# Kernel optimization log

Hardware: AMD Instinct MI355X
Metric: run time of the kernel (lower is better)

The kernel has to match this reference:

```python
import jax, jax.numpy as jnp
import numpy as np

M = 262144          # rows of A == prod(out_shape) == 512*512
N = 262144          # cols of A == prod(x.shape)
NNZ = 8388608       # 32 nonzeros per row on average
OUT_SHAPE = (512, 512)


def setup_inputs() -> dict:
    key = jax.random.key(0)
    k1, k2, k3, k4 = jax.random.split(key, 4)
    A_rows = jax.random.randint(k1, (NNZ,), 0, M, dtype=jnp.int32)
    A_cols = jax.random.randint(k2, (NNZ,), 0, N, dtype=jnp.int32)
    A_vals = jax.random.normal(k3, (NNZ,), dtype=jnp.float32)
    x = jax.random.normal(k4, OUT_SHAPE, dtype=jnp.float32)
    return {"x": x, "A_vals": A_vals, "A_rows": A_rows, "A_cols": A_cols}


def reference(x, A_vals, A_rows, A_cols):
    # x.reshape(A.shape[1], 1); torch.sparse.mm(A, x); reshape(out_shape)
    xf = x.reshape(-1)                                   # [N]
    contrib = A_vals * jnp.take(xf, A_cols)              # [NNZ] gather + multiply
    y = jax.ops.segment_sum(contrib, A_rows, num_segments=M)  # scatter-add over rows
    return y.reshape(OUT_SHAPE).astype(jnp.float32)
```

## Files before the change

### kernel.cpp

```cpp
#include <hip/hip_runtime.h>


#define BINS         32
#define ROW_SHIFT    13
#define ROWS_PER_BIN 8192
#define ENT          4096
#define CUR_STRIDE   32
#define SLICES       16

typedef int   __attribute__((ext_vector_type(4))) i32x4;
typedef float __attribute__((ext_vector_type(4))) f32x4;


__global__ __launch_bounds__(256) void zero_out_kernel(float* __restrict__ y, int n) {
    int i = blockIdx.x * blockDim.x + threadIdx.x;
    if (i < n) y[i] = 0.0f;
}

__global__ __launch_bounds__(256) void spmv_coo_scatter(
    const float* __restrict__ vals, const int* __restrict__ rows,
    const int* __restrict__ cols, const float* __restrict__ x,
    float* __restrict__ y, int nnz)
{
    int i = (blockIdx.x * blockDim.x + threadIdx.x) * 4;
    if (i + 3 < nnz) {
        float4 v = *reinterpret_cast<const float4*>(vals + i);
        int4   r = *reinterpret_cast<const int4*>(rows + i);
        int4   c = *reinterpret_cast<const int4*>(cols + i);
        atomicAdd(&y[r.x], v.x * x[c.x]);
        atomicAdd(&y[r.y], v.y * x[c.y]);
        atomicAdd(&y[r.z], v.z * x[c.z]);
        atomicAdd(&y[r.w], v.w * x[c.w]);
    } else {
        for (; i < nnz; ++i) atomicAdd(&y[rows[i]], vals[i] * x[cols[i]]);
    }
}


__global__ __launch_bounds__(256) void init_cursors(unsigned* __restrict__ gcur, int n) {
    int i = blockIdx.x * 256 + threadIdx.x;
    if (i < n) gcur[i] = 0u;
}

__global__ __launch_bounds__(256) void scatter2_kernel(
    const int*   __restrict__ rows, const int* __restrict__ cols,
    const float* __restrict__ vals, const float* __restrict__ x, int nnz,
    unsigned* __restrict__ gcur, unsigned cap,
    unsigned short* __restrict__ okeys, float* __restrict__ ocontrib)
{
    __shared__ unsigned cnt[BINS];
    __shared__ int      dstb[BINS];
    __shared__ unsigned cur2[BINS];
    __shared__ unsigned total_s;
    __shared__ unsigned short skey[ENT];
    __shared__ float          sval[ENT];
    __shared__ unsigned char  sbin[ENT];

    const int t = threadIdx.x;
    if (t < BINS) cnt[t] = 0u;
    __syncthreads();

    const int seg = blockIdx.x * ENT;

    int   rr[16];
    int   cc[16];
    float ff[16];

    if (seg + ENT <= nnz) {
        #pragma unroll
        for (int ch = 0; ch < 4; ++ch) {
            int base = seg + ch * 1024 + t * 4;
            i32x4 r4 = *reinterpret_cast<const i32x4*>(rows + base);
            i32x4 c4 = *reinterpret_cast<const i32x4*>(cols + base);
            f32x4 v4 = *reinterpret_cast<const f32x4*>(vals + base);
            rr[ch*4+0] = r4.x; cc[ch*4+0] = c4.x; ff[ch*4+0] = v4.x;
            rr[ch*4+1] = r4.y; cc[ch*4+1] = c4.y; ff[ch*4+1] = v4.y;
            rr[ch*4+2] = r4.z; cc[ch*4+2] = c4.z; ff[ch*4+2] = v4.z;
            rr[ch*4+3] = r4.w; cc[ch*4+3] = c4.w; ff[ch*4+3] = v4.w;
        }
        #pragma unroll
        for (int j = 0; j < 16; ++j) ff[j] *= x[cc[j]];
    } else {
        #pragma unroll
        for (int ch = 0; ch < 4; ++ch) {
            #pragma unroll
            for (int j = 0; j < 4; ++j) {
                int idx = seg + ch * 1024 + t * 4 + j;
                if (idx < nnz) { rr[ch*4+j] = rows[idx]; cc[ch*4+j] = cols[idx]; ff[ch*4+j] = vals[idx]; }
                else           { rr[ch*4+j] = -1; cc[ch*4+j] = 0; ff[ch*4+j] = 0.0f; }
            }
        }
        #pragma unroll
        for (int j = 0; j < 16; ++j) if (rr[j] >= 0) ff[j] *= x[cc[j]];
    }

    #pragma unroll
    for (int j = 0; j < 16; ++j)
        if (rr[j] >= 0) atomicAdd(&cnt[rr[j] >> ROW_SHIFT], 1u);
    __syncthreads();

    if (t < BINS) {
        unsigned c = cnt[t];
        unsigned resv = atomicAdd(&gcur[t * CUR_STRIDE], c);
        unsigned v = c;
        #pragma unroll
        for (int d = 1; d < BINS; d <<= 1) {
            unsigned o = __shfl_up(v, d, 64);
            if (t >= d) v += o;
        }
        unsigned ls = v - c;
        cur2[t] = ls;
        dstb[t] = (int)resv - (int)ls;
        if (t == BINS - 1) total_s = v;
    }
    __syncthreads();

    #pragma unroll
    for (int j = 0; j < 16; ++j) {
        if (rr[j] >= 0) {
            int b = rr[j] >> ROW_SHIFT;
            unsigned p = atomicAdd(&cur2[b], 1u);
            skey[p] = (unsigned short)(rr[j] & (ROWS_PER_BIN - 1));
            sval[p] = ff[j];
            sbin[p] = (unsigned char)b;
        }
    }
    __syncthreads();

    const unsigned total = total_s;
    for (unsigned i = t; i < total; i += 256) {
        int b = sbin[i];
        unsigned off = (unsigned)(dstb[b] + (int)i);
        if (off < cap) {
            size_t dst = (size_t)b * cap + off;
            okeys[dst]    = skey[i];
            ocontrib[dst] = sval[i];
        }
    }
}

__global__ __launch_bounds__(512) void accum2_kernel(
    const unsigned short* __restrict__ okeys, const float* __restrict__ ocontrib,
    const unsigned* __restrict__ gcur, unsigned cap,
    float* __restrict__ partials)
{
    __shared__ float acc[ROWS_PER_BIN];
    const int t   = threadIdx.x;
    const int bin = blockIdx.x / SLICES;
    const int sl  = blockIdx.x - bin * SLICES;

    float4 z = make_float4(0.f, 0.f, 0.f, 0.f);
    #pragma unroll
    for (int i = 0; i < ROWS_PER_BIN / (512 * 4); ++i)
        *reinterpret_cast<float4*>(&acc[(i * 512 + t) * 4]) = z;
    __syncthreads();

    unsigned count = gcur[bin * CUR_STRIDE];
    if (count > cap) count = cap;
    unsigned chunk = ((count + SLICES - 1u) / SLICES + 3u) & ~3u;
    unsigned lo = (unsigned)sl * chunk;
    unsigned hi = lo + chunk; if (hi > count) hi = count;

    const unsigned short* k = okeys    + (size_t)bin * cap;
    const float*          c = ocontrib + (size_t)bin * cap;

    unsigned i = lo + (unsigned)t * 4u;

    for (; i + 6147u < hi; i += 8192u) {
        ushort4 k0 = *reinterpret_cast<const ushort4*>(k + i);
        ushort4 k1 = *reinterpret_cast<const ushort4*>(k + i + 2048u);
        ushort4 k2 = *reinterpret_cast<const ushort4*>(k + i + 4096u);
        ushort4 k3 = *reinterpret_cast<const ushort4*>(k + i + 6144u);
        float4  c0 = *reinterpret_cast<const float4*>(c + i);
        float4  c1 = *reinterpret_cast<const float4*>(c + i + 2048u);
        float4  c2 = *reinterpret_cast<const float4*>(c + i + 4096u);
        float4  c3 = *reinterpret_cast<const float4*>(c + i + 6144u);
        atomicAdd(&acc[k0.x], c0.x); atomicAdd(&acc[k0.y], c0.y);
        atomicAdd(&acc[k0.z], c0.z); atomicAdd(&acc[k0.w], c0.w);
        atomicAdd(&acc[k1.x], c1.x); atomicAdd(&acc[k1.y], c1.y);
        atomicAdd(&acc[k1.z], c1.z); atomicAdd(&acc[k1.w], c1.w);
        atomicAdd(&acc[k2.x], c2.x); atomicAdd(&acc[k2.y], c2.y);
        atomicAdd(&acc[k2.z], c2.z); atomicAdd(&acc[k2.w], c2.w);
        atomicAdd(&acc[k3.x], c3.x); atomicAdd(&acc[k3.y], c3.y);
        atomicAdd(&acc[k3.z], c3.z); atomicAdd(&acc[k3.w], c3.w);
    }
    for (; i + 3u < hi; i += 2048u) {
        ushort4 k4 = *reinterpret_cast<const ushort4*>(k + i);
        float4  c4 = *reinterpret_cast<const float4*>(c + i);
        atomicAdd(&acc[k4.x], c4.x);
        atomicAdd(&acc[k4.y], c4.y);
        atomicAdd(&acc[k4.z], c4.z);
        atomicAdd(&acc[k4.w], c4.w);
    }
    for (; i < hi; ++i) atomicAdd(&acc[k[i]], c[i]);
    __syncthreads();

    float* p = partials + (size_t)blockIdx.x * ROWS_PER_BIN;
    #pragma unroll
    for (int i2 = 0; i2 < ROWS_PER_BIN / (512 * 4); ++i2) {
        int l = (i2 * 512 + t) * 4;
        *reinterpret_cast<float4*>(p + l) = *reinterpret_cast<const float4*>(&acc[l]);
    }
}

__global__ __launch_bounds__(256) void reduce2_kernel(
    const float* __restrict__ partials, float* __restrict__ y, int out_size)
{
    int r0 = (blockIdx.x * 256 + threadIdx.x) * 4;
    if (r0 >= out_size) return;
    int bin = r0 >> ROW_SHIFT, local = r0 & (ROWS_PER_BIN - 1);
    const float* p = partials + ((size_t)bin * SLICES) * ROWS_PER_BIN + local;
    float4 s = make_float4(0.f, 0.f, 0.f, 0.f);
    #pragma unroll
    for (int j = 0; j < SLICES; ++j) {
        float4 v = *reinterpret_cast<const float4*>(p + (size_t)j * ROWS_PER_BIN);
        s.x += v.x; s.y += v.y; s.z += v.z; s.w += v.w;
    }
    *reinterpret_cast<float4*>(y + r0) = s;
}

extern "C" void kernel_launch(void* const* d_in, const int* in_sizes, int n_in,
                              void* d_out, int out_size, void* d_ws, size_t ws_size,
                              hipStream_t stream) {
    const float* x    = (const float*)d_in[0];
    const float* vals = (const float*)d_in[1];
    const int*   rows = (const int*)d_in[2];
    const int*   cols = (const int*)d_in[3];
    float* y = (float*)d_out;

    const int nnz  = in_sizes[1];
    const int bins = (out_size + ROWS_PER_BIN - 1) / ROWS_PER_BIN;

    unsigned cap = (unsigned)(nnz / (bins > 0 ? bins : 1)) + 16384u;
    cap = (cap + 3u) & ~3u;

    auto align256 = [](size_t v) { return (v + 255) & ~(size_t)255; };

    size_t off_contrib  = 0;
    size_t off_keys     = align256(off_contrib + (size_t)BINS * cap * 4);
    size_t off_partials = align256(off_keys + (size_t)BINS * cap * 2);
    size_t off_gcur     = align256(off_partials + (size_t)BINS * SLICES * ROWS_PER_BIN * 4);
    size_t need         = align256(off_gcur + (size_t)BINS * CUR_STRIDE * 4);

    const bool ok = (bins == BINS) && (need <= ws_size) && (nnz > 0) &&
                    (out_size == BINS * ROWS_PER_BIN);

    if (!ok) {
        zero_out_kernel<<<(out_size + 255) / 256, 256, 0, stream>>>(y, out_size);
        spmv_coo_scatter<<<(nnz + 1023) / 1024, 256, 0, stream>>>(vals, rows, cols, x, y, nnz);
        return;
    }

    char* w = (char*)d_ws;
    float*          ocontrib = (float*)(w + off_contrib);
    unsigned short* okeys    = (unsigned short*)(w + off_keys);
    float*          partials = (float*)(w + off_partials);
    unsigned*       gcur     = (unsigned*)(w + off_gcur);

    const int ncur = BINS * CUR_STRIDE;
    init_cursors<<<(ncur + 255) / 256, 256, 0, stream>>>(gcur, ncur);
    scatter2_kernel<<<(nnz + ENT - 1) / ENT, 256, 0, stream>>>(
        rows, cols, vals, x, nnz, gcur, cap, okeys, ocontrib);
    accum2_kernel<<<BINS * SLICES, 512, 0, stream>>>(okeys, ocontrib, gcur, cap, partials);
    reduce2_kernel<<<(out_size / 4 + 255) / 256, 256, 0, stream>>>(partials, y, out_size);
}
```

Baseline: 217.3 us.

## Fuse scatter, accumulate and reduce into one persistent kernel with grid barriers

Replaces the three separate kernels (bin scatter, per-bin shared-memory accumulation, partial reduction) with a single persistent kernel of BINS*SL blocks that loops over segments, then uses software grid-wide barriers between phases. The shared-memory staging buffer and the accumulator are placed in a union. Slices per bin rise from 16 to 32 when the workspace allows. This removes launch gaps and tail effects between stages. In exchange, the grid is capped at 1024 blocks of 256 threads for the scatter phase, the spin barrier depends on all blocks being co-resident, and the accumulate phase now runs with 256 threads per block instead of 512. The final reduce is scalar and sums 32 partials per output.

```diff
diff --git a/kernel.cpp b/kernel.cpp
--- a/kernel.cpp
+++ b/kernel.cpp
@@ -6,10 +6,9 @@
 #define ROWS_PER_BIN 8192
 #define ENT          4096
 #define CUR_STRIDE   32
-#define SLICES       16
-
-typedef int   __attribute__((ext_vector_type(4))) i32x4;
-typedef float __attribute__((ext_vector_type(4))) f32x4;
+
+typedef int   i32x4 __attribute__((ext_vector_type(4)));
+typedef float f32x4 __attribute__((ext_vector_type(4)));
 
 
 __global__ __launch_bounds__(256) void zero_out_kernel(float* __restrict__ y, int n) {
@@ -37,186 +36,214 @@
 }
 
 
-__global__ __launch_bounds__(256) void init_cursors(unsigned* __restrict__ gcur, int n) {
+__global__ __launch_bounds__(256) void init_kernel(
+    unsigned* __restrict__ gcur, int ncur, unsigned* __restrict__ bar)
+{
     int i = blockIdx.x * 256 + threadIdx.x;
-    if (i < n) gcur[i] = 0u;
-}
-
-__global__ __launch_bounds__(256) void scatter2_kernel(
+    if (i < ncur) gcur[i] = 0u;
+    if (blockIdx.x == 0 && threadIdx.x < 2) bar[threadIdx.x] = 0u;
+}
+
+__device__ __forceinline__ void grid_sync(unsigned* bar, unsigned nb) {
+    __syncthreads();
+    if (threadIdx.x == 0) {
+        __threadfence();
+        unsigned g = __hip_atomic_load(&bar[1], __ATOMIC_RELAXED, __HIP_MEMORY_SCOPE_AGENT);
+        unsigned a = __hip_atomic_fetch_add(&bar[0], 1u, __ATOMIC_ACQ_REL, __HIP_MEMORY_SCOPE_AGENT);
+        if (a + 1u == nb) {
+            __hip_atomic_store(&bar[0], 0u, __ATOMIC_RELAXED, __HIP_MEMORY_SCOPE_AGENT);
+            __hip_atomic_fetch_add(&bar[1], 1u, __ATOMIC_RELEASE, __HIP_MEMORY_SCOPE_AGENT);
+        } else {
+            while (__hip_atomic_load(&bar[1], __ATOMIC_ACQUIRE, __HIP_MEMORY_SCOPE_AGENT) == g)
+                __builtin_amdgcn_s_sleep(8);
+        }
+        __threadfence();
+    }
+    __syncthreads();
+}
+
+template <int SL>
+__global__ __launch_bounds__(256, 4) void mega_kernel(
     const int*   __restrict__ rows, const int* __restrict__ cols,
     const float* __restrict__ vals, const float* __restrict__ x, int nnz,
     unsigned* __restrict__ gcur, unsigned cap,
-    unsigned short* __restrict__ okeys, float* __restrict__ ocontrib)
+    unsigned short* __restrict__ okeys, float* __restrict__ ocontrib,
+    float* __restrict__ partials, float* __restrict__ y,
+    unsigned* __restrict__ bar, int out_size)
 {
-    __shared__ unsigned cnt[BINS];
-    __shared__ int      dstb[BINS];
-    __shared__ unsigned cur2[BINS];
-    __shared__ unsigned total_s;
-    __shared__ unsigned short skey[ENT];
-    __shared__ float          sval[ENT];
-    __shared__ unsigned char  sbin[ENT];
-
-    const int t = threadIdx.x;
-    if (t < BINS) cnt[t] = 0u;
-    __syncthreads();
-
-    const int seg = blockIdx.x * ENT;
-
-    int   rr[16];
-    int   cc[16];
-    float ff[16];
-
-    if (seg + ENT <= nnz) {
+    __shared__ union {
+        struct {
+            unsigned short skey[ENT];
+            float          sval[ENT];
+            unsigned char  sbin[ENT];
+            unsigned cnt[BINS];
+            int      dstb[BINS];
+            unsigned cur2[BINS];
+            unsigned total;
+        } s;
+        float acc[ROWS_PER_BIN];
+    } sm;
+
+    const int t    = threadIdx.x;
+    const int blk  = blockIdx.x;
+    const int grid = BINS * SL;
+    const int nseg = (nnz + ENT - 1) / ENT;
+
+    for (int s = blk; s < nseg; s += grid) {
+        __syncthreads();
+        if (t < BINS) sm.s.cnt[t] = 0u;
+        __syncthreads();
+
+        const int seg = s * ENT;
+        int   rr[16];
+        int   cc[16];
+        float ff[16];
+
+        if (seg + ENT <= nnz) {
+            #pragma unroll
+            for (int ch = 0; ch < 4; ++ch) {
+                int base = seg + ch * 1024 + t * 4;
+                i32x4 r4 = *reinterpret_cast<const i32x4*>(rows + base);
+                i32x4 c4 = *reinterpret_cast<const i32x4*>(cols + base);
+                f32x4 v4 = *reinterpret_cast<const f32x4*>(vals + base);
+                rr[ch*4+0] = r4.x; cc[ch*4+0] = c4.x; ff[ch*4+0] = v4.x;
+                rr[ch*4+1] = r4.y; cc[ch*4+1] = c4.y; ff[ch*4+1] = v4.y;
+                rr[ch*4+2] = r4.z; cc[ch*4+2] = c4.z; ff[ch*4+2] = v4.z;
+                rr[ch*4+3] = r4.w; cc[ch*4+3] = c4.w; ff[ch*4+3] = v4.w;
+            }
+            #pragma unroll
+            for (int j = 0; j < 16; ++j) ff[j] *= x[cc[j]];
+        } else {
+            #pragma unroll
+            for (int ch = 0; ch < 4; ++ch) {
+                #pragma unroll
+                for (int j = 0; j < 4; ++j) {
+                    int idx = seg + ch * 1024 + t * 4 + j;
+                    if (idx < nnz) { rr[ch*4+j] = rows[idx]; cc[ch*4+j] = cols[idx]; ff[ch*4+j] = vals[idx]; }
+                    else           { rr[ch*4+j] = -1; cc[ch*4+j] = 0; ff[ch*4+j] = 0.0f; }
+                }
+            }
+            #pragma unroll
+            for (int j = 0; j < 16; ++j) if (rr[j] >= 0) ff[j] *= x[cc[j]];
+        }
+
         #pragma unroll
-        for (int ch = 0; ch < 4; ++ch) {
-            int base = seg + ch * 1024 + t * 4;
-            i32x4 r4 = *reinterpret_cast<const i32x4*>(rows + base);
-            i32x4 c4 = *reinterpret_cast<const i32x4*>(cols + base);
-            f32x4 v4 = *reinterpret_cast<const f32x4*>(vals + base);
-            rr[ch*4+0] = r4.x; cc[ch*4+0] = c4.x; ff[ch*4+0] = v4.x;
-            rr[ch*4+1] = r4.y; cc[ch*4+1] = c4.y; ff[ch*4+1] = v4.y;
-            rr[ch*4+2] = r4.z; cc[ch*4+2] = c4.z; ff[ch*4+2] = v4.z;
-            rr[ch*4+3] = r4.w; cc[ch*4+3] = c4.w; ff[ch*4+3] = v4.w;
-        }
+        for (int j = 0; j < 16; ++j)
+            if (rr[j] >= 0) atomicAdd(&sm.s.cnt[rr[j] >> ROW_SHIFT], 1u);
+        __syncthreads();
+
+        if (t < BINS) {
+            unsigned c = sm.s.cnt[t];
+            unsigned resv = atomicAdd(&gcur[t * CUR_STRIDE], c);
+            unsigned v = c;
+            #pragma unroll
+            for (int d = 1; d < BINS; d <<= 1) {
+                unsigned o = __shfl_up(v, d, 64);
+                if (t >= d) v += o;
+            }
+            unsigned ls = v - c;
+            sm.s.cur2[t] = ls;
+            sm.s.dstb[t] = (int)resv - (int)ls;
+            if (t == BINS - 1) sm.s.total = v;
+        }
+        __syncthreads();
+
         #pragma unroll
-        for (int j = 0; j < 16; ++j) ff[j] *= x[cc[j]];
-    } else {
+        for (int j = 0; j < 16; ++j) {
+            if (rr[j] >= 0) {
+                int b = rr[j] >> ROW_SHIFT;
+                unsigned p = atomicAdd(&sm.s.cur2[b], 1u);
+                sm.s.skey[p] = (unsigned short)(rr[j] & (ROWS_PER_BIN - 1));
+                sm.s.sval[p] = ff[j];
+                sm.s.sbin[p] = (unsigned char)b;
+            }
+        }
+        __syncthreads();
+
+        const unsigned total = sm.s.total;
+        for (unsigned i = t; i < total; i += 256) {
+            int b = sm.s.sbin[i];
+            unsigned off = (unsigned)(sm.s.dstb[b] + (int)i);
+            if (off < cap) {
+                size_t dst = (size_t)b * cap + off;
+                okeys[dst]    = sm.s.skey[i];
+                ocontrib[dst] = sm.s.sval[i];
+            }
+        }
+    }
+
+    grid_sync(bar, (unsigned)grid);
+
+    {
+        const int bin = blk / SL;
+        const int sl  = blk - bin * SL;
+
+        float4 z = make_float4(0.f, 0.f, 0.f, 0.f);
         #pragma unroll
-        for (int ch = 0; ch < 4; ++ch) {
-            #pragma unroll
-            for (int j = 0; j < 4; ++j) {
-                int idx = seg + ch * 1024 + t * 4 + j;
-                if (idx < nnz) { rr[ch*4+j] = rows[idx]; cc[ch*4+j] = cols[idx]; ff[ch*4+j] = vals[idx]; }
-                else           { rr[ch*4+j] = -1; cc[ch*4+j] = 0; ff[ch*4+j] = 0.0f; }
-            }
-        }
+        for (int i = 0; i < ROWS_PER_BIN / (256 * 4); ++i)
+            *reinterpret_cast<float4*>(&sm.acc[(i * 256 + t) * 4]) = z;
+        __syncthreads();
+
+        unsigned count = gcur[bin * CUR_STRIDE];
+        if (count > cap) count = cap;
+        unsigned chunk = ((count + (unsigned)SL - 1u) / (unsigned)SL + 3u) & ~3u;
+        unsigned lo = (unsigned)sl * chunk;
+        unsigned hi = lo + chunk; if (hi > count) hi = count;
+
+        const unsigned short* k = okeys    + (size_t)bin * cap;
+        const float*          c = ocontrib + (size_t)bin * cap;
+
+        unsigned i = lo + (unsigned)t * 4u;
+
+        for (; i + 7171u < hi; i += 8192u) {
+            ushort4 K[8];
+            float4  C[8];
+            #pragma unroll
+            for (int j = 0; j < 8; ++j) K[j] = *reinterpret_cast<const ushort4*>(k + i + (unsigned)j * 1024u);
+            #pragma unroll
+            for (int j = 0; j < 8; ++j) C[j] = *reinterpret_cast<const float4*>(c + i + (unsigned)j * 1024u);
+            #pragma unroll
+            for (int j = 0; j < 8; ++j) {
+                atomicAdd(&sm.acc[K[j].x], C[j].x);
+                atomicAdd(&sm.acc[K[j].y], C[j].y);
+                atomicAdd(&sm.acc[K[j].z], C[j].z);
+                atomicAdd(&sm.acc[K[j].w], C[j].w);
+            }
+        }
+        for (; i + 3u < hi; i += 1024u) {
+            ushort4 k4 = *reinterpret_cast<const ushort4*>(k + i);
+            float4  c4 = *reinterpret_cast<const float4*>(c + i);
+            atomicAdd(&sm.acc[k4.x], c4.x);
+            atomicAdd(&sm.acc[k4.y], c4.y);
+            atomicAdd(&sm.acc[k4.z], c4.z);
+            atomicAdd(&sm.acc[k4.w], c4.w);
+        }
+        for (; i < hi; ++i) atomicAdd(&sm.acc[k[i]], c[i]);
+        __syncthreads();
+
+        float* p = partials + (size_t)blk * ROWS_PER_BIN;
         #pragma unroll
-        for (int j = 0; j < 16; ++j) if (rr[j] >= 0) ff[j] *= x[cc[j]];
-    }
-
-    #pragma unroll
-    for (int j = 0; j < 16; ++j)
-        if (rr[j] >= 0) atomicAdd(&cnt[rr[j] >> ROW_SHIFT], 1u);
-    __syncthreads();
-
-    if (t < BINS) {
-        unsigned c = cnt[t];
-        unsigned resv = atomicAdd(&gcur[t * CUR_STRIDE], c);
-        unsigned v = c;
-        #pragma unroll
-        for (int d = 1; d < BINS; d <<= 1) {
-            unsigned o = __shfl_up(v, d, 64);
-            if (t >= d) v += o;
-        }
-        unsigned ls = v - c;
-        cur2[t] = ls;
-        dstb[t] = (int)resv - (int)ls;
-        if (t == BINS - 1) total_s = v;
-    }
-    __syncthreads();
-
-    #pragma unroll
-    for (int j = 0; j < 16; ++j) {
-        if (rr[j] >= 0) {
-            int b = rr[j] >> ROW_SHIFT;
-            unsigned p = atomicAdd(&cur2[b], 1u);
-            skey[p] = (unsigned short)(rr[j] & (ROWS_PER_BIN - 1));
-            sval[p] = ff[j];
-            sbin[p] = (unsigned char)b;
-        }
-    }
-    __syncthreads();
-
-    const unsigned total = total_s;
-    for (unsigned i = t; i < total; i += 256) {
-        int b = sbin[i];
-        unsigned off = (unsigned)(dstb[b] + (int)i);
-        if (off < cap) {
-            size_t dst = (size_t)b * cap + off;
-            okeys[dst]    = skey[i];
-            ocontrib[dst] = sval[i];
-        }
-    }
-}
-
-__global__ __launch_bounds__(512) void accum2_kernel(
-    const unsigned short* __restrict__ okeys, const float* __restrict__ ocontrib,
-    const unsigned* __restrict__ gcur, unsigned cap,
-    float* __restrict__ partials)
-{
-    __shared__ float acc[ROWS_PER_BIN];
-    const int t   = threadIdx.x;
-    const int bin = blockIdx.x / SLICES;
-    const int sl  = blockIdx.x - bin * SLICES;
-
-    float4 z = make_float4(0.f, 0.f, 0.f, 0.f);
-    #pragma unroll
-    for (int i = 0; i < ROWS_PER_BIN / (512 * 4); ++i)
-        *reinterpret_cast<float4*>(&acc[(i * 512 + t) * 4]) = z;
-    __syncthreads();
-
-    unsigned count = gcur[bin * CUR_STRIDE];
-    if (count > cap) count = cap;
-    unsigned chunk = ((count + SLICES - 1u) / SLICES + 3u) & ~3u;
-    unsigned lo = (unsigned)sl * chunk;
-    unsigned hi = lo + chunk; if (hi > count) hi = count;
-
-    const unsigned short* k = okeys    + (size_t)bin * cap;
-    const float*          c = ocontrib + (size_t)bin * cap;
-
-    unsigned i = lo + (unsigned)t * 4u;
-
-    for (; i + 6147u < hi; i += 8192u) {
-        ushort4 k0 = *reinterpret_cast<const ushort4*>(k + i);
-        ushort4 k1 = *reinterpret_cast<const ushort4*>(k + i + 2048u);
-        ushort4 k2 = *reinterpret_cast<const ushort4*>(k + i + 4096u);
-        ushort4 k3 = *reinterpret_cast<const ushort4*>(k + i + 6144u);
-        float4  c0 = *reinterpret_cast<const float4*>(c + i);
-        float4  c1 = *reinterpret_cast<const float4*>(c + i + 2048u);
-        float4  c2 = *reinterpret_cast<const float4*>(c + i + 4096u);
-        float4  c3 = *reinterpret_cast<const float4*>(c + i + 6144u);
-        atomicAdd(&acc[k0.x], c0.x); atomicAdd(&acc[k0.y], c0.y);
-        atomicAdd(&acc[k0.z], c0.z); atomicAdd(&acc[k0.w], c0.w);
-        atomicAdd(&acc[k1.x], c1.x); atomicAdd(&acc[k1.y], c1.y);
-        atomicAdd(&acc[k1.z], c1.z); atomicAdd(&acc[k1.w], c1.w);
-        atomicAdd(&acc[k2.x], c2.x); atomicAdd(&acc[k2.y], c2.y);
-        atomicAdd(&acc[k2.z], c2.z); atomicAdd(&acc[k2.w], c2.w);
-        atomicAdd(&acc[k3.x], c3.x); atomicAdd(&acc[k3.y], c3.y);
-        atomicAdd(&acc[k3.z], c3.z); atomicAdd(&acc[k3.w], c3.w);
-    }
-    for (; i + 3u < hi; i += 2048u) {
-        ushort4 k4 = *reinterpret_cast<const ushort4*>(k + i);
-        float4  c4 = *reinterpret_cast<const float4*>(c + i);
-        atomicAdd(&acc[k4.x], c4.x);
-        atomicAdd(&acc[k4.y], c4.y);
-        atomicAdd(&acc[k4.z], c4.z);
-        atomicAdd(&acc[k4.w], c4.w);
-    }
-    for (; i < hi; ++i) atomicAdd(&acc[k[i]], c[i]);
-    __syncthreads();
-
-    float* p = partials + (size_t)blockIdx.x * ROWS_PER_BIN;
-    #pragma unroll
-    for (int i2 = 0; i2 < ROWS_PER_BIN / (512 * 4); ++i2) {
-        int l = (i2 * 512 + t) * 4;
-        *reinterpret_cast<float4*>(p + l) = *reinterpret_cast<const float4*>(&acc[l]);
-    }
-}
-
-__global__ __launch_bounds__(256) void reduce2_kernel(
-    const float* __restrict__ partials, float* __restrict__ y, int out_size)
-{
-    int r0 = (blockIdx.x * 256 + threadIdx.x) * 4;
-    if (r0 >= out_size) return;
-    int bin = r0 >> ROW_SHIFT, local = r0 & (ROWS_PER_BIN - 1);
-    const float* p = partials + ((size_t)bin * SLICES) * ROWS_PER_BIN + local;
-    float4 s = make_float4(0.f, 0.f, 0.f, 0.f);
-    #pragma unroll
-    for (int j = 0; j < SLICES; ++j) {
-        float4 v = *reinterpret_cast<const float4*>(p + (size_t)j * ROWS_PER_BIN);
-        s.x += v.x; s.y += v.y; s.z += v.z; s.w += v.w;
-    }
-    *reinterpret_cast<float4*>(y + r0) = s;
+        for (int i2 = 0; i2 < ROWS_PER_BIN / (256 * 4); ++i2) {
+            int l = (i2 * 256 + t) * 4;
+            *reinterpret_cast<float4*>(p + l) = *reinterpret_cast<const float4*>(&sm.acc[l]);
+        }
+    }
+
+    grid_sync(bar, (unsigned)grid);
+
+    {
+        const int rpb = out_size / grid;
+        const int r0  = blk * rpb;
+        for (int r = r0 + t; r < r0 + rpb; r += 256) {
+            int bin   = r >> ROW_SHIFT;
+            int local = r & (ROWS_PER_BIN - 1);
+            const float* p = partials + ((size_t)bin * SL) * ROWS_PER_BIN + local;
+            float ssum = 0.0f;
+            #pragma unroll
+            for (int j = 0; j < SL; ++j) ssum += p[(size_t)j * ROWS_PER_BIN];
+            y[r] = ssum;
+        }
+    }
 }
 
 extern "C" void kernel_launch(void* const* d_in, const int* in_sizes, int n_in,
@@ -236,11 +263,18 @@
 
     auto align256 = [](size_t v) { return (v + 255) & ~(size_t)255; };
 
-    size_t off_contrib  = 0;
-    size_t off_keys     = align256(off_contrib + (size_t)BINS * cap * 4);
-    size_t off_partials = align256(off_keys + (size_t)BINS * cap * 2);
-    size_t off_gcur     = align256(off_partials + (size_t)BINS * SLICES * ROWS_PER_BIN * 4);
-    size_t need         = align256(off_gcur + (size_t)BINS * CUR_STRIDE * 4);
+    int slices = 32;
+    size_t off_contrib = 0, off_keys = 0, off_partials = 0, off_gcur = 0, off_bar = 0, need = 0;
+    for (int attempt = 0; attempt < 2; ++attempt) {
+        off_contrib  = 0;
+        off_keys     = align256(off_contrib + (size_t)BINS * cap * 4);
+        off_partials = align256(off_keys + (size_t)BINS * cap * 2);
+        off_gcur     = align256(off_partials + (size_t)BINS * slices * ROWS_PER_BIN * 4);
+        off_bar      = align256(off_gcur + (size_t)BINS * CUR_STRIDE * 4);
+        need         = align256(off_bar + 256);
+        if (need <= ws_size) break;
+        slices = 16;
+    }
 
     const bool ok = (bins == BINS) && (need <= ws_size) && (nnz > 0) &&
                     (out_size == BINS * ROWS_PER_BIN);
@@ -256,11 +290,16 @@
     unsigned short* okeys    = (unsigned short*)(w + off_keys);
     float*          partials = (float*)(w + off_partials);
     unsigned*       gcur     = (unsigned*)(w + off_gcur);
+    unsigned*       bar      = (unsigned*)(w + off_bar);
 
     const int ncur = BINS * CUR_STRIDE;
-    init_cursors<<<(ncur + 255) / 256, 256, 0, stream>>>(gcur, ncur);
-    scatter2_kernel<<<(nnz + ENT - 1) / ENT, 256, 0, stream>>>(
-        rows, cols, vals, x, nnz, gcur, cap, okeys, ocontrib);
-    accum2_kernel<<<BINS * SLICES, 512, 0, stream>>>(okeys, ocontrib, gcur, cap, partials);
-    reduce2_kernel<<<(out_size / 4 + 255) / 256, 256, 0, stream>>>(partials, y, out_size);
-}
+    init_kernel<<<(ncur + 255) / 256, 256, 0, stream>>>(gcur, ncur, bar);
+
+    if (slices == 32) {
+        mega_kernel<32><<<BINS * 32, 256, 0, stream>>>(
+            rows, cols, vals, x, nnz, gcur, cap, okeys, ocontrib, partials, y, bar, out_size);
+    } else {
+        mega_kernel<16><<<BINS * 16, 256, 0, stream>>>(
+            rows, cols, vals, x, nnz, gcur, cap, okeys, ocontrib, partials, y, bar, out_size);
+    }
+}
```

New measurement: 715.8 us. 3.29x slower.

## Use 256 fine row bins with 4 slices and block-wide scan

Applied to the files above, without the earlier changes.

Raises the row-bin count from 32 to 256, so each bin spans 1024 rows and one block-level LDS histogram covers 256 bins. This needs a block-wide two-level scan across four wavefronts instead of a single-wave scan. The accumulation kernel now uses 4 slices per bin with a 4 KB LDS accumulator, which cuts partial-sum traffic and reduce work and should allow higher occupancy. Input loads are marked nontemporal. In exchange the scatter writes to global memory become more fragmented across 256 destinations, and the smaller cap margin raises the risk of overflow on skewed inputs.

```diff
diff --git a/kernel.cpp b/kernel.cpp
--- a/kernel.cpp
+++ b/kernel.cpp
@@ -1,15 +1,15 @@
 #include <hip/hip_runtime.h>
 
 
-#define BINS         32
-#define ROW_SHIFT    13
-#define ROWS_PER_BIN 8192
+#define BINS         256
+#define ROW_SHIFT    10
+#define ROWS_PER_BIN 1024
 #define ENT          4096
 #define CUR_STRIDE   32
-#define SLICES       16
-
-typedef int   __attribute__((ext_vector_type(4))) i32x4;
-typedef float __attribute__((ext_vector_type(4))) f32x4;
+#define SL           4
+
+typedef int   i32x4 __attribute__((ext_vector_type(4)));
+typedef float f32x4 __attribute__((ext_vector_type(4)));
 
 
 __global__ __launch_bounds__(256) void zero_out_kernel(float* __restrict__ y, int n) {
@@ -48,16 +48,16 @@
     unsigned* __restrict__ gcur, unsigned cap,
     unsigned short* __restrict__ okeys, float* __restrict__ ocontrib)
 {
-    __shared__ unsigned cnt[BINS];
-    __shared__ int      dstb[BINS];
-    __shared__ unsigned cur2[BINS];
-    __shared__ unsigned total_s;
     __shared__ unsigned short skey[ENT];
     __shared__ float          sval[ENT];
     __shared__ unsigned char  sbin[ENT];
+    __shared__ int      cnt_dstb[BINS];
+    __shared__ unsigned cur2[BINS];
+    __shared__ unsigned wsum[4];
+    __shared__ unsigned total_s;
 
     const int t = threadIdx.x;
-    if (t < BINS) cnt[t] = 0u;
+    cnt_dstb[t] = 0;
     __syncthreads();
 
     const int seg = blockIdx.x * ENT;
@@ -70,9 +70,9 @@
         #pragma unroll
         for (int ch = 0; ch < 4; ++ch) {
             int base = seg + ch * 1024 + t * 4;
-            i32x4 r4 = *reinterpret_cast<const i32x4*>(rows + base);
-            i32x4 c4 = *reinterpret_cast<const i32x4*>(cols + base);
-            f32x4 v4 = *reinterpret_cast<const f32x4*>(vals + base);
+            i32x4 r4 = __builtin_nontemporal_load(reinterpret_cast<const i32x4*>(rows + base));
+            i32x4 c4 = __builtin_nontemporal_load(reinterpret_cast<const i32x4*>(cols + base));
+            f32x4 v4 = __builtin_nontemporal_load(reinterpret_cast<const f32x4*>(vals + base));
             rr[ch*4+0] = r4.x; cc[ch*4+0] = c4.x; ff[ch*4+0] = v4.x;
             rr[ch*4+1] = r4.y; cc[ch*4+1] = c4.y; ff[ch*4+1] = v4.y;
             rr[ch*4+2] = r4.z; cc[ch*4+2] = c4.z; ff[ch*4+2] = v4.z;
@@ -96,24 +96,30 @@
 
     #pragma unroll
     for (int j = 0; j < 16; ++j)
-        if (rr[j] >= 0) atomicAdd(&cnt[rr[j] >> ROW_SHIFT], 1u);
-    __syncthreads();
-
-    if (t < BINS) {
-        unsigned c = cnt[t];
-        unsigned resv = atomicAdd(&gcur[t * CUR_STRIDE], c);
+        if (rr[j] >= 0) atomicAdd((unsigned*)&cnt_dstb[rr[j] >> ROW_SHIFT], 1u);
+    __syncthreads();
+
+    {
+        unsigned c = (unsigned)cnt_dstb[t];
+        unsigned r = atomicAdd(&gcur[t * CUR_STRIDE], c);
         unsigned v = c;
-        #pragma unroll
-        for (int d = 1; d < BINS; d <<= 1) {
+        const int lane = t & 63, wave = t >> 6;
+        #pragma unroll
+        for (int d = 1; d < 64; d <<= 1) {
             unsigned o = __shfl_up(v, d, 64);
-            if (t >= d) v += o;
-        }
-        unsigned ls = v - c;
-        cur2[t] = ls;
-        dstb[t] = (int)resv - (int)ls;
-        if (t == BINS - 1) total_s = v;
-    }
-    __syncthreads();
+            if (lane >= d) v += o;
+        }
+        if (lane == 63) wsum[wave] = v;
+        __syncthreads();
+        unsigned base = 0;
+        #pragma unroll
+        for (int w2 = 0; w2 < 3; ++w2) base += (w2 < wave) ? wsum[w2] : 0u;
+        unsigned excl = base + v - c;
+        cur2[t]     = excl;
+        cnt_dstb[t] = (int)r - (int)excl;
+        if (t == 255) total_s = base + v;
+        __syncthreads();
+    }
 
     #pragma unroll
     for (int j = 0; j < 16; ++j) {
@@ -130,7 +136,7 @@
     const unsigned total = total_s;
     for (unsigned i = t; i < total; i += 256) {
         int b = sbin[i];
-        unsigned off = (unsigned)(dstb[b] + (int)i);
+        unsigned off = (unsigned)(cnt_dstb[b] + (int)i);
         if (off < cap) {
             size_t dst = (size_t)b * cap + off;
             okeys[dst]    = skey[i];
@@ -146,18 +152,16 @@
 {
     __shared__ float acc[ROWS_PER_BIN];
     const int t   = threadIdx.x;
-    const int bin = blockIdx.x / SLICES;
-    const int sl  = blockIdx.x - bin * SLICES;
-
-    float4 z = make_float4(0.f, 0.f, 0.f, 0.f);
-    #pragma unroll
-    for (int i = 0; i < ROWS_PER_BIN / (512 * 4); ++i)
-        *reinterpret_cast<float4*>(&acc[(i * 512 + t) * 4]) = z;
+    const int bin = blockIdx.x >> 2;
+    const int sl  = blockIdx.x & 3;
+
+    if (t < ROWS_PER_BIN) acc[t] = 0.0f;
+    acc[t + 512] = 0.0f;
     __syncthreads();
 
     unsigned count = gcur[bin * CUR_STRIDE];
     if (count > cap) count = cap;
-    unsigned chunk = ((count + SLICES - 1u) / SLICES + 3u) & ~3u;
+    unsigned chunk = ((count + (unsigned)SL - 1u) / (unsigned)SL + 3u) & ~3u;
     unsigned lo = (unsigned)sl * chunk;
     unsigned hi = lo + chunk; if (hi > count) hi = count;
 
@@ -167,22 +171,19 @@
     unsigned i = lo + (unsigned)t * 4u;
 
     for (; i + 6147u < hi; i += 8192u) {
-        ushort4 k0 = *reinterpret_cast<const ushort4*>(k + i);
-        ushort4 k1 = *reinterpret_cast<const ushort4*>(k + i + 2048u);
-        ushort4 k2 = *reinterpret_cast<const ushort4*>(k + i + 4096u);
-        ushort4 k3 = *reinterpret_cast<const ushort4*>(k + i + 6144u);
-        float4  c0 = *reinterpret_cast<const float4*>(c + i);
-        float4  c1 = *reinterpret_cast<const float4*>(c + i + 2048u);
-        float4  c2 = *reinterpret_cast<const float4*>(c + i + 4096u);
-        float4  c3 = *reinterpret_cast<const float4*>(c + i + 6144u);
-        atomicAdd(&acc[k0.x], c0.x); atomicAdd(&acc[k0.y], c0.y);
-        atomicAdd(&acc[k0.z], c0.z); atomicAdd(&acc[k0.w], c0.w);
-        atomicAdd(&acc[k1.x], c1.x); atomicAdd(&acc[k1.y], c1.y);
-        atomicAdd(&acc[k1.z], c1.z); atomicAdd(&acc[k1.w], c1.w);
-        atomicAdd(&acc[k2.x], c2.x); atomicAdd(&acc[k2.y], c2.y);
-        atomicAdd(&acc[k2.z], c2.z); atomicAdd(&acc[k2.w], c2.w);
-        atomicAdd(&acc[k3.x], c3.x); atomicAdd(&acc[k3.y], c3.y);
-        atomicAdd(&acc[k3.z], c3.z); atomicAdd(&acc[k3.w], c3.w);
+        ushort4 K[4];
+        float4  C[4];
+        #pragma unroll
+        for (int j = 0; j < 4; ++j) K[j] = *reinterpret_cast<const ushort4*>(k + i + (unsigned)j * 2048u);
+        #pragma unroll
+        for (int j = 0; j < 4; ++j) C[j] = *reinterpret_cast<const float4*>(c + i + (unsigned)j * 2048u);
+        #pragma unroll
+        for (int j = 0; j < 4; ++j) {
+            atomicAdd(&acc[K[j].x], C[j].x);
+            atomicAdd(&acc[K[j].y], C[j].y);
+            atomicAdd(&acc[K[j].z], C[j].z);
+            atomicAdd(&acc[K[j].w], C[j].w);
+        }
     }
     for (; i + 3u < hi; i += 2048u) {
         ushort4 k4 = *reinterpret_cast<const ushort4*>(k + i);
@@ -196,11 +197,8 @@
     __syncthreads();
 
     float* p = partials + (size_t)blockIdx.x * ROWS_PER_BIN;
-    #pragma unroll
-    for (int i2 = 0; i2 < ROWS_PER_BIN / (512 * 4); ++i2) {
-        int l = (i2 * 512 + t) * 4;
-        *reinterpret_cast<float4*>(p + l) = *reinterpret_cast<const float4*>(&acc[l]);
-    }
+    p[t]       = acc[t];
+    p[t + 512] = acc[t + 512];
 }
 
 __global__ __launch_bounds__(256) void reduce2_kernel(
@@ -209,10 +207,10 @@
     int r0 = (blockIdx.x * 256 + threadIdx.x) * 4;
     if (r0 >= out_size) return;
     int bin = r0 >> ROW_SHIFT, local = r0 & (ROWS_PER_BIN - 1);
-    const float* p = partials + ((size_t)bin * SLICES) * ROWS_PER_BIN + local;
+    const float* p = partials + ((size_t)bin * SL) * ROWS_PER_BIN + local;
     float4 s = make_float4(0.f, 0.f, 0.f, 0.f);
     #pragma unroll
-    for (int j = 0; j < SLICES; ++j) {
+    for (int j = 0; j < SL; ++j) {
         float4 v = *reinterpret_cast<const float4*>(p + (size_t)j * ROWS_PER_BIN);
         s.x += v.x; s.y += v.y; s.z += v.z; s.w += v.w;
     }
@@ -231,7 +229,7 @@
     const int nnz  = in_sizes[1];
     const int bins = (out_size + ROWS_PER_BIN - 1) / ROWS_PER_BIN;
 
-    unsigned cap = (unsigned)(nnz / (bins > 0 ? bins : 1)) + 16384u;
+    unsigned cap = (unsigned)(nnz / (bins > 0 ? bins : 1)) + 4096u;
     cap = (cap + 3u) & ~3u;
 
     auto align256 = [](size_t v) { return (v + 255) & ~(size_t)255; };
@@ -239,7 +237,7 @@
     size_t off_contrib  = 0;
     size_t off_keys     = align256(off_contrib + (size_t)BINS * cap * 4);
     size_t off_partials = align256(off_keys + (size_t)BINS * cap * 2);
-    size_t off_gcur     = align256(off_partials + (size_t)BINS * SLICES * ROWS_PER_BIN * 4);
+    size_t off_gcur     = align256(off_partials + (size_t)BINS * SL * ROWS_PER_BIN * 4);
     size_t need         = align256(off_gcur + (size_t)BINS * CUR_STRIDE * 4);
 
     const bool ok = (bins == BINS) && (need <= ws_size) && (nnz > 0) &&
@@ -261,6 +259,6 @@
     init_cursors<<<(ncur + 255) / 256, 256, 0, stream>>>(gcur, ncur);
     scatter2_kernel<<<(nnz + ENT - 1) / ENT, 256, 0, stream>>>(
         rows, cols, vals, x, nnz, gcur, cap, okeys, ocontrib);
-    accum2_kernel<<<BINS * SLICES, 512, 0, stream>>>(okeys, ocontrib, gcur, cap, partials);
+    accum2_kernel<<<BINS * SL, 512, 0, stream>>>(okeys, ocontrib, gcur, cap, partials);
     reduce2_kernel<<<(out_size / 4 + 255) / 256, 256, 0, stream>>>(partials, y, out_size);
 }
```

Measured after the change: 247.4 us. 13.8% more time.

## Fuse slice reduction into accumulate kernel via last-block done counter

Applied to the files above, without the earlier changes.

Removes the separate reduce kernel. Each bin's last-finishing slice block, found through an atomic done counter with fences, sums the 16 partial slices straight into y. The cursor-init kernel is also replaced with a single hipMemsetAsync that clears both the cursors and the done counters. This saves two kernel launches, but the reduction now runs on only 32 blocks instead of many, which may leave the tail of the kernel poorly parallelised.

```diff
diff --git a/kernel.cpp b/kernel.cpp
--- a/kernel.cpp
+++ b/kernel.cpp
@@ -6,10 +6,10 @@
 #define ROWS_PER_BIN 8192
 #define ENT          4096
 #define CUR_STRIDE   32
-#define SLICES       16
-
-typedef int   __attribute__((ext_vector_type(4))) i32x4;
-typedef float __attribute__((ext_vector_type(4))) f32x4;
+#define SL           16
+
+typedef int   i32x4 __attribute__((ext_vector_type(4)));
+typedef float f32x4 __attribute__((ext_vector_type(4)));
 
 
 __global__ __launch_bounds__(256) void zero_out_kernel(float* __restrict__ y, int n) {
@@ -37,11 +37,6 @@
 }
 
 
-__global__ __launch_bounds__(256) void init_cursors(unsigned* __restrict__ gcur, int n) {
-    int i = blockIdx.x * 256 + threadIdx.x;
-    if (i < n) gcur[i] = 0u;
-}
-
 __global__ __launch_bounds__(256) void scatter2_kernel(
     const int*   __restrict__ rows, const int* __restrict__ cols,
     const float* __restrict__ vals, const float* __restrict__ x, int nnz,
@@ -139,15 +134,17 @@
     }
 }
 
-__global__ __launch_bounds__(512) void accum2_kernel(
+__global__ __launch_bounds__(512) void accum_fused_kernel(
     const unsigned short* __restrict__ okeys, const float* __restrict__ ocontrib,
     const unsigned* __restrict__ gcur, unsigned cap,
-    float* __restrict__ partials)
+    float* __restrict__ partials, unsigned* __restrict__ donec,
+    float* __restrict__ y)
 {
     __shared__ float acc[ROWS_PER_BIN];
+    __shared__ unsigned last_s;
     const int t   = threadIdx.x;
-    const int bin = blockIdx.x / SLICES;
-    const int sl  = blockIdx.x - bin * SLICES;
+    const int bin = blockIdx.x / SL;
+    const int sl  = blockIdx.x - bin * SL;
 
     float4 z = make_float4(0.f, 0.f, 0.f, 0.f);
     #pragma unroll
@@ -157,7 +154,7 @@
 
     unsigned count = gcur[bin * CUR_STRIDE];
     if (count > cap) count = cap;
-    unsigned chunk = ((count + SLICES - 1u) / SLICES + 3u) & ~3u;
+    unsigned chunk = ((count + (unsigned)SL - 1u) / (unsigned)SL + 3u) & ~3u;
     unsigned lo = (unsigned)sl * chunk;
     unsigned hi = lo + chunk; if (hi > count) hi = count;
 
@@ -167,22 +164,19 @@
     unsigned i = lo + (unsigned)t * 4u;
 
     for (; i + 6147u < hi; i += 8192u) {
-        ushort4 k0 = *reinterpret_cast<const ushort4*>(k + i);
-        ushort4 k1 = *reinterpret_cast<const ushort4*>(k + i + 2048u);
-        ushort4 k2 = *reinterpret_cast<const ushort4*>(k + i + 4096u);
-        ushort4 k3 = *reinterpret_cast<const ushort4*>(k + i + 6144u);
-        float4  c0 = *reinterpret_cast<const float4*>(c + i);
-        float4  c1 = *reinterpret_cast<const float4*>(c + i + 2048u);
-        float4  c2 = *reinterpret_cast<const float4*>(c + i + 4096u);
-        float4  c3 = *reinterpret_cast<const float4*>(c + i + 6144u);
-        atomicAdd(&acc[k0.x], c0.x); atomicAdd(&acc[k0.y], c0.y);
-        atomicAdd(&acc[k0.z], c0.z); atomicAdd(&acc[k0.w], c0.w);
-        atomicAdd(&acc[k1.x], c1.x); atomicAdd(&acc[k1.y], c1.y);
-        atomicAdd(&acc[k1.z], c1.z); atomicAdd(&acc[k1.w], c1.w);
-        atomicAdd(&acc[k2.x], c2.x); atomicAdd(&acc[k2.y], c2.y);
-        atomicAdd(&acc[k2.z], c2.z); atomicAdd(&acc[k2.w], c2.w);
-        atomicAdd(&acc[k3.x], c3.x); atomicAdd(&acc[k3.y], c3.y);
-        atomicAdd(&acc[k3.z], c3.z); atomicAdd(&acc[k3.w], c3.w);
+        ushort4 K[4];
+        float4  C[4];
+        #pragma unroll
+        for (int j = 0; j < 4; ++j) K[j] = *reinterpret_cast<const ushort4*>(k + i + (unsigned)j * 2048u);
+        #pragma unroll
+        for (int j = 0; j < 4; ++j) C[j] = *reinterpret_cast<const float4*>(c + i + (unsigned)j * 2048u);
+        #pragma unroll
+        for (int j = 0; j < 4; ++j) {
+            atomicAdd(&acc[K[j].x], C[j].x);
+            atomicAdd(&acc[K[j].y], C[j].y);
+            atomicAdd(&acc[K[j].z], C[j].z);
+            atomicAdd(&acc[K[j].w], C[j].w);
+        }
     }
     for (; i + 3u < hi; i += 2048u) {
         ushort4 k4 = *reinterpret_cast<const ushort4*>(k + i);
@@ -201,22 +195,31 @@
         int l = (i2 * 512 + t) * 4;
         *reinterpret_cast<float4*>(p + l) = *reinterpret_cast<const float4*>(&acc[l]);
     }
-}
-
-__global__ __launch_bounds__(256) void reduce2_kernel(
-    const float* __restrict__ partials, float* __restrict__ y, int out_size)
-{
-    int r0 = (blockIdx.x * 256 + threadIdx.x) * 4;
-    if (r0 >= out_size) return;
-    int bin = r0 >> ROW_SHIFT, local = r0 & (ROWS_PER_BIN - 1);
-    const float* p = partials + ((size_t)bin * SLICES) * ROWS_PER_BIN + local;
-    float4 s = make_float4(0.f, 0.f, 0.f, 0.f);
-    #pragma unroll
-    for (int j = 0; j < SLICES; ++j) {
-        float4 v = *reinterpret_cast<const float4*>(p + (size_t)j * ROWS_PER_BIN);
-        s.x += v.x; s.y += v.y; s.z += v.z; s.w += v.w;
-    }
-    *reinterpret_cast<float4*>(y + r0) = s;
+
+    __syncthreads();
+    if (t == 0) {
+        __threadfence();
+        unsigned d = __hip_atomic_fetch_add(&donec[bin * CUR_STRIDE], 1u,
+                                            __ATOMIC_ACQ_REL, __HIP_MEMORY_SCOPE_AGENT);
+        last_s = (d == (unsigned)(SL - 1)) ? 1u : 0u;
+    }
+    __syncthreads();
+    if (!last_s) return;
+    __threadfence();
+
+    const float* pb = partials + (size_t)bin * SL * ROWS_PER_BIN;
+    float* yb = y + (size_t)bin * ROWS_PER_BIN;
+    #pragma unroll
+    for (int blk2 = 0; blk2 < ROWS_PER_BIN / (512 * 4); ++blk2) {
+        int r0 = (blk2 * 512 + t) * 4;
+        float4 s = make_float4(0.f, 0.f, 0.f, 0.f);
+        #pragma unroll
+        for (int j = 0; j < SL; ++j) {
+            float4 v = *reinterpret_cast<const float4*>(pb + (size_t)j * ROWS_PER_BIN + r0);
+            s.x += v.x; s.y += v.y; s.z += v.z; s.w += v.w;
+        }
+        *reinterpret_cast<float4*>(yb + r0) = s;
+    }
 }
 
 extern "C" void kernel_launch(void* const* d_in, const int* in_sizes, int n_in,
@@ -239,8 +242,9 @@
     size_t off_contrib  = 0;
     size_t off_keys     = align256(off_contrib + (size_t)BINS * cap * 4);
     size_t off_partials = align256(off_keys + (size_t)BINS * cap * 2);
-    size_t off_gcur     = align256(off_partials + (size_t)BINS * SLICES * ROWS_PER_BIN * 4);
-    size_t need         = align256(off_gcur + (size_t)BINS * CUR_STRIDE * 4);
+    size_t off_gcur     = align256(off_partials + (size_t)BINS * SL * ROWS_PER_BIN * 4);
+    size_t off_done     = off_gcur + (size_t)BINS * CUR_STRIDE * 4;
+    size_t need         = align256(off_done + (size_t)BINS * CUR_STRIDE * 4);
 
     const bool ok = (bins == BINS) && (need <= ws_size) && (nnz > 0) &&
                     (out_size == BINS * ROWS_PER_BIN);
@@ -256,11 +260,12 @@
     unsigned short* okeys    = (unsigned short*)(w + off_keys);
     float*          partials = (float*)(w + off_partials);
     unsigned*       gcur     = (unsigned*)(w + off_gcur);
-
-    const int ncur = BINS * CUR_STRIDE;
-    init_cursors<<<(ncur + 255) / 256, 256, 0, stream>>>(gcur, ncur);
+    unsigned*       donec    = (unsigned*)(w + off_done);
+
+    hipMemsetAsync(gcur, 0, (size_t)2 * BINS * CUR_STRIDE * 4, stream);
+
     scatter2_kernel<<<(nnz + ENT - 1) / ENT, 256, 0, stream>>>(
         rows, cols, vals, x, nnz, gcur, cap, okeys, ocontrib);
-    accum2_kernel<<<BINS * SLICES, 512, 0, stream>>>(okeys, ocontrib, gcur, cap, partials);
-    reduce2_kernel<<<(out_size / 4 + 255) / 256, 256, 0, stream>>>(partials, y, out_size);
-}
+    accum_fused_kernel<<<BINS * SL, 512, 0, stream>>>(
+        okeys, ocontrib, gcur, cap, partials, donec, y);
+}
```

Result: slower. 254.8 us (+17.2%).
